# Optimization experiments

Measured on AMD Instinct MI355X. Metric: run time of the kernel, lower is better.

## Reference

```python
import jax, jax.numpy as jnp
import numpy as np

TEMPERATURE = 0.07
EPS = 1e-12  # F.normalize default eps


def setup_inputs() -> dict:
    key = jax.random.key(0)
    k1, k2, k3 = jax.random.split(key, 3)
    B, C, H, W = 2, 128, 256, 256
    return {
        "z1": jax.random.normal(k1, (B, C, H, W), dtype=jnp.float32),
        "z2": jax.random.normal(k2, (B, C, H, W), dtype=jnp.float32),
        "labels": jax.random.randint(k3, (B, H, W), 0, 5),
        "chunks": 64,
    }


def _l2_normalize(x, axis):
    n = jnp.sqrt(jnp.sum(x * x, axis=axis, keepdims=True))
    return x / jnp.maximum(n, EPS)


def reference(z1, z2, labels, chunks):
    B, C, H, W = z1.shape
    N = H * W
    M = N // chunks  # chunk length (N divisible by chunks)

    # normalize over channel dim, flatten spatial, split into chunks: [B, C, K, M]
    z1c = _l2_normalize(z1, axis=1).reshape(B, C, N).reshape(B, C, chunks, M)
    z2c = _l2_normalize(z2, axis=1).reshape(B, C, N).reshape(B, C, chunks, M)
    lab = labels.reshape(B, N).reshape(B, chunks, M)  # [B, K, M]

    # positives: cosine sim between matching chunks of z1 and z2 (unit vectors -> dot)
    pos = jnp.einsum("bckm,bckm->bkm", z1c, z2c) / TEMPERATURE  # [B, K, M]

    # negatives: in the source, (reps2, l2) after the j-loop are the LAST chunk of z2
    reps2_last = z2c[:, :, -1, :]  # [B, C, M]
    l2_last = lab[:, -1, :]        # [B, M]

    neg = jnp.einsum("bckm,bcn->bkmn", z1c, reps2_last)  # [B, K, M, M]
    mask = (lab[:, :, :, None] != l2_last[:, None, None, :])  # True where labels differ
    neg = neg * mask / TEMPERATURE

    logits = jnp.concatenate([pos[..., None], neg], axis=-1)  # [B, K, M, M+1]
    logp = jax.nn.log_softmax(logits, axis=-1)

    # per-(b,chunk) term is -mean over [M, M+1]; final is mean over B*chunks terms
    return -jnp.mean(logp)
```

## Files before the change

kernel.cpp:

```cpp
#include <hip/hip_runtime.h>
#include <hip/hip_bf16.h>

constexpr int BB = 2;
constexpr int CC = 128;
constexpr int NN = 65536;
constexpr int MM = 1024;
constexpr int LASTOFF = 63 * 1024;
constexpr float INV_T = 1.0f / 0.07f;
constexpr float L2E = 1.44269504088896340736f;
constexpr float C2 = INV_T * L2E;
constexpr float SCALE = 1.0f / (134348800.0f * 1.44269504088896340736f);

typedef float f32x4 __attribute__((ext_vector_type(4)));
typedef short bf16x8 __attribute__((ext_vector_type(8)));

__device__ __forceinline__ uint pack_bf16(float a, float b) {
  __hip_bfloat16 ha = __float2bfloat16(a);
  __hip_bfloat16 hb = __float2bfloat16(b);
  ushort ua = *reinterpret_cast<ushort*>(&ha);
  ushort ub = *reinterpret_cast<ushort*>(&hb);
  return (uint)ua | ((uint)ub << 16);
}

__global__ __launch_bounds__(256) void k_prep(
    const float* __restrict__ z1, const float* __restrict__ z2,
    uint* __restrict__ z1n, float* __restrict__ posv) {
  __shared__ float t1[64 * 129];
  __shared__ float part[3][8][65];
  __shared__ float inv1s[64];
  const int b = blockIdx.y;
  const int p0 = blockIdx.x * 64;
  const int t = threadIdx.x;
  const int p2 = t & 31;
  const int q = t >> 5;
  const float* s1 = z1 + (size_t)b * CC * NN + p0 + 2 * p2;
  const float* s2 = z2 + (size_t)b * CC * NN + p0 + 2 * p2;
  float a11 = 0.f, a22 = 0.f, a12 = 0.f;
  float b11 = 0.f, b22 = 0.f, b12 = 0.f;
#pragma unroll
  for (int e = 0; e < 16; e++) {
    int c = e * 8 + q;
    float2 x = *reinterpret_cast<const float2*>(s1 + (size_t)c * NN);
    float2 y = *reinterpret_cast<const float2*>(s2 + (size_t)c * NN);
    t1[(2 * p2) * 129 + c] = x.x;
    t1[(2 * p2 + 1) * 129 + c] = x.y;
    a11 += x.x * x.x; a22 += y.x * y.x; a12 += x.x * y.x;
    b11 += x.y * x.y; b22 += y.y * y.y; b12 += x.y * y.y;
  }
  part[0][q][2 * p2] = a11; part[0][q][2 * p2 + 1] = b11;
  part[1][q][2 * p2] = a22; part[1][q][2 * p2 + 1] = b22;
  part[2][q][2 * p2] = a12; part[2][q][2 * p2 + 1] = b12;
  __syncthreads();
  if (t < 64) {
    float s11 = 0.f, s22 = 0.f, s12 = 0.f;
#pragma unroll
    for (int qq = 0; qq < 8; qq++) {
      s11 += part[0][qq][t];
      s22 += part[1][qq][t];
      s12 += part[2][qq][t];
    }
    float i1 = 1.0f / fmaxf(sqrtf(s11), 1e-12f);
    float i2 = 1.0f / fmaxf(sqrtf(s22), 1e-12f);
    inv1s[t] = i1;
    posv[(size_t)b * NN + p0 + t] = s12 * i1 * i2 * INV_T;
  }
  __syncthreads();
  const size_t obase = ((size_t)b * NN + p0) * 64;
#pragma unroll
  for (int e = 0; e < 16; e++) {
    int lin = e * 256 + t;
    int pp = lin >> 6;
    int cp = lin & 63;
    float i1 = inv1s[pp];
    float v0 = t1[pp * 129 + 2 * cp] * i1;
    float v1 = t1[pp * 129 + 2 * cp + 1] * i1;
    z1n[obase + (size_t)pp * 64 + cp] = pack_bf16(v0, v1);
  }
}

__global__ __launch_bounds__(256) void k_r2(
    const float* __restrict__ z2, uint* __restrict__ r2n) {
  __shared__ float t2[64 * 129];
  __shared__ float part[8][65];
  __shared__ float inv2s[64];
  const int b = blockIdx.y;
  const int pg = blockIdx.x * 64;
  const int p0 = LASTOFF + pg;
  const int t = threadIdx.x;
  const int p2 = t & 31;
  const int q = t >> 5;
  const float* s2 = z2 + (size_t)b * CC * NN + p0 + 2 * p2;
  float a22 = 0.f, b22 = 0.f;
#pragma unroll
  for (int e = 0; e < 16; e++) {
    int c = e * 8 + q;
    float2 y = *reinterpret_cast<const float2*>(s2 + (size_t)c * NN);
    t2[(2 * p2) * 129 + c] = y.x;
    t2[(2 * p2 + 1) * 129 + c] = y.y;
    a22 += y.x * y.x;
    b22 += y.y * y.y;
  }
  part[q][2 * p2] = a22;
  part[q][2 * p2 + 1] = b22;
  __syncthreads();
  if (t < 64) {
    float s22 = 0.f;
#pragma unroll
    for (int qq = 0; qq < 8; qq++) s22 += part[qq][t];
    inv2s[t] = 1.0f / fmaxf(sqrtf(s22), 1e-12f);
  }
  __syncthreads();
  const size_t obase = ((size_t)b * MM + pg) * 64;
#pragma unroll
  for (int e = 0; e < 16; e++) {
    int lin = e * 256 + t;
    int pp = lin >> 6;
    int cp = lin & 63;
    float i2 = inv2s[pp];
    float v0 = t2[pp * 129 + 2 * cp] * i2;
    float v1 = t2[pp * 129 + 2 * cp + 1] * i2;
    r2n[obase + (size_t)pp * 64 + cp] = pack_bf16(v0, v1);
  }
}

__global__ __launch_bounds__(256, 2) void k_gemm(
    const ushort* __restrict__ z1n,
    const ushort* __restrict__ r2n,
    const int* __restrict__ lab,
    const float* __restrict__ posv,
    float* __restrict__ accum) {
  const int b = blockIdx.y;
  const int tid = threadIdx.x;
  const int w = tid >> 6;
  const int lane = tid & 63;
  const int r = lane & 15;
  const int kg = lane >> 4;
  const int wrow0 = blockIdx.x * 256 + w * 64;

  const ushort* Abase = z1n + ((size_t)b * NN + wrow0) * CC;
  bf16x8 av[4][4];
#pragma unroll
  for (int g = 0; g < 4; g++)
#pragma unroll
    for (int kk = 0; kk < 4; kk++)
      av[g][kk] = *reinterpret_cast<const bf16x8*>(
          Abase + ((size_t)(g * 16 + r)) * CC + kg * 8 + kk * 32);

  int rl[16];
#pragma unroll
  for (int g = 0; g < 4; g++)
#pragma unroll
    for (int i = 0; i < 4; i++)
      rl[g * 4 + i] = lab[(size_t)b * NN + wrow0 + g * 16 + kg * 4 + i];

  float sAcc[16], xAcc[16];
#pragma unroll
  for (int s = 0; s < 16; s++) { sAcc[s] = 0.f; xAcc[s] = 0.f; }

  const ushort* Bbase = r2n + (size_t)b * MM * CC;
  const int* clbase = lab + (size_t)b * NN + LASTOFF;

#pragma unroll 1
  for (int ch = 0; ch < 16; ch++) {
    const int n0 = ch * 64;
    bf16x8 bv[4][4];
#pragma unroll
    for (int tt = 0; tt < 4; tt++)
#pragma unroll
      for (int kk = 0; kk < 4; kk++)
        bv[tt][kk] = *reinterpret_cast<const bf16x8*>(
            Bbase + ((size_t)(n0 + tt * 16 + r)) * CC + kg * 8 + kk * 32);
    int cl[4];
#pragma unroll
    for (int tt = 0; tt < 4; tt++)
      cl[tt] = clbase[n0 + tt * 16 + r];

    f32x4 acc[4][4];
#pragma unroll
    for (int g = 0; g < 4; g++)
#pragma unroll
      for (int tt = 0; tt < 4; tt++)
        acc[g][tt] = f32x4{0.f, 0.f, 0.f, 0.f};

#pragma unroll
    for (int kk = 0; kk < 4; kk++)
#pragma unroll
      for (int g = 0; g < 4; g++)
#pragma unroll
        for (int tt = 0; tt < 4; tt++)
          acc[g][tt] = __builtin_amdgcn_mfma_f32_16x16x32_bf16(
              av[g][kk], bv[tt][kk], acc[g][tt], 0, 0, 0);

#pragma unroll
    for (int g = 0; g < 4; g++)
#pragma unroll
      for (int tt = 0; tt < 4; tt++)
#pragma unroll
        for (int i = 0; i < 4; i++) {
          float xm = acc[g][tt][i] * C2;
          float e = exp2f(xm);
          bool sel = (rl[g * 4 + i] != cl[tt]);
          sAcc[g * 4 + i] += sel ? e : 1.0f;
          xAcc[g * 4 + i] += sel ? xm : 0.0f;
        }
  }

#pragma unroll
  for (int d = 1; d < 16; d <<= 1) {
#pragma unroll
    for (int s = 0; s < 16; s++) {
      sAcc[s] += __shfl_xor(sAcc[s], d);
      xAcc[s] += __shfl_xor(xAcc[s], d);
    }
  }

  float tv = 0.f;
  if (r == 0) {
#pragma unroll
    for (int g = 0; g < 4; g++)
#pragma unroll
      for (int i = 0; i < 4; i++) {
        int row = wrow0 + g * 16 + kg * 4 + i;
        float pv = posv[(size_t)b * NN + row] * L2E;
        float s = sAcc[g * 4 + i] + exp2f(pv);
        float x = xAcc[g * 4 + i] + pv;
        tv += 1025.0f * __log2f(s) - x;
      }
  }
  tv += __shfl_xor(tv, 16);
  tv += __shfl_xor(tv, 32);
  if (lane == 0) atomicAdd(accum, tv);
}

__global__ void k_final(const float* __restrict__ accum, float* __restrict__ out) {
  out[0] = accum[0] * SCALE;
}

extern "C" void kernel_launch(void* const* d_in, const int* in_sizes, int n_in,
                              void* d_out, int out_size, void* d_ws, size_t ws_size,
                              hipStream_t stream) {
  const float* z1 = (const float*)d_in[0];
  const float* z2 = (const float*)d_in[1];
  const int* lab = (const int*)d_in[2];

  char* ws = (char*)d_ws;
  uint* z1n = (uint*)ws;
  uint* r2n = (uint*)(ws + 33554432);
  float* posv = (float*)(ws + 34078720);
  float* accum = (float*)(ws + 34603008);

  hipMemsetAsync(accum, 0, sizeof(float), stream);

  k_prep<<<dim3(NN / 64, BB), 256, 0, stream>>>(z1, z2, z1n, posv);
  k_r2<<<dim3(MM / 64, BB), 256, 0, stream>>>(z2, r2n);
  k_gemm<<<dim3(NN / 256, BB), 256, 0, stream>>>(
      (const ushort*)z1n, (const ushort*)r2n, lab, posv, accum);
  k_final<<<1, 1, 0, stream>>>(accum, (float*)d_out);
}
```

Measured before the change: 256.1 us.

## Normalize z1 inside GEMM and compute masked logit sum via per-label class sums

The bf16 normalized z1 buffer is dropped. A lighter k_pos kernel now computes only the inverse norms and positive logits, and k_gemm reads raw z1, normalizes and transposes it through LDS itself. The per-row sum of masked negative logits is computed algebraically: each class gets a precomputed z2 sum vector over columns with a different label, and one small extra MFMA multiplies it by the row, replacing the per-element xAcc accumulation. The inner loop also folds the temperature scale into the norms and uses the raw exp2 intrinsic. This removes a large intermediate write/read and some per-element ALU work, at the cost of a bigger LDS footprint in the GEMM, lower occupancy, and some bf16 rounding of the class sums.

```diff
diff --git a/kernel.cpp b/kernel.cpp
--- a/kernel.cpp
+++ b/kernel.cpp
@@ -10,6 +10,7 @@
 constexpr float L2E = 1.44269504088896340736f;
 constexpr float C2 = INV_T * L2E;
 constexpr float SCALE = 1.0f / (134348800.0f * 1.44269504088896340736f);
+constexpr float EPSN = 1e-12f;
 
 typedef float f32x4 __attribute__((ext_vector_type(4)));
 typedef short bf16x8 __attribute__((ext_vector_type(8)));
@@ -22,67 +23,39 @@
   return (uint)ua | ((uint)ub << 16);
 }
 
-__global__ __launch_bounds__(256) void k_prep(
+__global__ __launch_bounds__(256) void k_pos(
     const float* __restrict__ z1, const float* __restrict__ z2,
-    uint* __restrict__ z1n, float* __restrict__ posv) {
-  __shared__ float t1[64 * 129];
-  __shared__ float part[3][8][65];
-  __shared__ float inv1s[64];
+    float* __restrict__ i1c2, float* __restrict__ posv) {
   const int b = blockIdx.y;
-  const int p0 = blockIdx.x * 64;
-  const int t = threadIdx.x;
-  const int p2 = t & 31;
-  const int q = t >> 5;
-  const float* s1 = z1 + (size_t)b * CC * NN + p0 + 2 * p2;
-  const float* s2 = z2 + (size_t)b * CC * NN + p0 + 2 * p2;
-  float a11 = 0.f, a22 = 0.f, a12 = 0.f;
-  float b11 = 0.f, b22 = 0.f, b12 = 0.f;
-#pragma unroll
-  for (int e = 0; e < 16; e++) {
-    int c = e * 8 + q;
-    float2 x = *reinterpret_cast<const float2*>(s1 + (size_t)c * NN);
-    float2 y = *reinterpret_cast<const float2*>(s2 + (size_t)c * NN);
-    t1[(2 * p2) * 129 + c] = x.x;
-    t1[(2 * p2 + 1) * 129 + c] = x.y;
-    a11 += x.x * x.x; a22 += y.x * y.x; a12 += x.x * y.x;
-    b11 += x.y * x.y; b22 += y.y * y.y; b12 += x.y * y.y;
-  }
-  part[0][q][2 * p2] = a11; part[0][q][2 * p2 + 1] = b11;
-  part[1][q][2 * p2] = a22; part[1][q][2 * p2 + 1] = b22;
-  part[2][q][2 * p2] = a12; part[2][q][2 * p2 + 1] = b12;
-  __syncthreads();
-  if (t < 64) {
-    float s11 = 0.f, s22 = 0.f, s12 = 0.f;
-#pragma unroll
-    for (int qq = 0; qq < 8; qq++) {
-      s11 += part[0][qq][t];
-      s22 += part[1][qq][t];
-      s12 += part[2][qq][t];
-    }
-    float i1 = 1.0f / fmaxf(sqrtf(s11), 1e-12f);
-    float i2 = 1.0f / fmaxf(sqrtf(s22), 1e-12f);
-    inv1s[t] = i1;
-    posv[(size_t)b * NN + p0 + t] = s12 * i1 * i2 * INV_T;
-  }
-  __syncthreads();
-  const size_t obase = ((size_t)b * NN + p0) * 64;
-#pragma unroll
-  for (int e = 0; e < 16; e++) {
-    int lin = e * 256 + t;
-    int pp = lin >> 6;
-    int cp = lin & 63;
-    float i1 = inv1s[pp];
-    float v0 = t1[pp * 129 + 2 * cp] * i1;
-    float v1 = t1[pp * 129 + 2 * cp + 1] * i1;
-    z1n[obase + (size_t)pp * 64 + cp] = pack_bf16(v0, v1);
-  }
+  const int px = blockIdx.x * 512 + 2 * threadIdx.x;
+  const float* p1 = z1 + (size_t)b * CC * NN + px;
+  const float* p2 = z2 + (size_t)b * CC * NN + px;
+  float s11a = 0.f, s22a = 0.f, s12a = 0.f;
+  float s11b = 0.f, s22b = 0.f, s12b = 0.f;
+#pragma unroll 8
+  for (int c = 0; c < CC; c++) {
+    float2 x = *reinterpret_cast<const float2*>(p1 + (size_t)c * NN);
+    float2 y = *reinterpret_cast<const float2*>(p2 + (size_t)c * NN);
+    s11a += x.x * x.x; s22a += y.x * y.x; s12a += x.x * y.x;
+    s11b += x.y * x.y; s22b += y.y * y.y; s12b += x.y * y.y;
+  }
+  float i1a = 1.0f / fmaxf(sqrtf(s11a), EPSN);
+  float i2a = 1.0f / fmaxf(sqrtf(s22a), EPSN);
+  float i1b = 1.0f / fmaxf(sqrtf(s11b), EPSN);
+  float i2b = 1.0f / fmaxf(sqrtf(s22b), EPSN);
+  float2 iv = {i1a * C2, i1b * C2};
+  float2 pv = {s12a * i1a * i2a * C2, s12b * i1b * i2b * C2};
+  *reinterpret_cast<float2*>(i1c2 + (size_t)b * NN + px) = iv;
+  *reinterpret_cast<float2*>(posv + (size_t)b * NN + px) = pv;
 }
 
 __global__ __launch_bounds__(256) void k_r2(
-    const float* __restrict__ z2, uint* __restrict__ r2n) {
+    const float* __restrict__ z2, const int* __restrict__ lab,
+    uint* __restrict__ r2n, float* __restrict__ Sv) {
   __shared__ float t2[64 * 129];
   __shared__ float part[8][65];
   __shared__ float inv2s[64];
+  __shared__ int cls[64];
   const int b = blockIdx.y;
   const int pg = blockIdx.x * 64;
   const int p0 = LASTOFF + pg;
@@ -107,7 +80,8 @@
     float s22 = 0.f;
 #pragma unroll
     for (int qq = 0; qq < 8; qq++) s22 += part[qq][t];
-    inv2s[t] = 1.0f / fmaxf(sqrtf(s22), 1e-12f);
+    inv2s[t] = 1.0f / fmaxf(sqrtf(s22), EPSN);
+    cls[t] = lab[(size_t)b * NN + p0 + t];
   }
   __syncthreads();
   const size_t obase = ((size_t)b * MM + pg) * 64;
@@ -121,41 +95,90 @@
     float v1 = t2[pp * 129 + 2 * cp + 1] * i2;
     r2n[obase + (size_t)pp * 64 + cp] = pack_bf16(v0, v1);
   }
-}
-
-__global__ __launch_bounds__(256, 2) void k_gemm(
-    const ushort* __restrict__ z1n,
-    const ushort* __restrict__ r2n,
-    const int* __restrict__ lab,
-    const float* __restrict__ posv,
+  const int c = t & 127;
+  const int h = t >> 7;
+  float tot = 0.f, se0 = 0.f, se1 = 0.f, se2 = 0.f, se3 = 0.f, se4 = 0.f;
+#pragma unroll
+  for (int k = 0; k < 32; k++) {
+    int pp = h * 32 + k;
+    float val = t2[pp * 129 + c] * inv2s[pp];
+    int lb = cls[pp];
+    tot += val;
+    se0 += (lb == 0) ? val : 0.f;
+    se1 += (lb == 1) ? val : 0.f;
+    se2 += (lb == 2) ? val : 0.f;
+    se3 += (lb == 3) ? val : 0.f;
+    se4 += (lb == 4) ? val : 0.f;
+  }
+  float* svb = Sv + b * 640 + c;
+  atomicAdd(svb + 0 * 128, tot - se0);
+  atomicAdd(svb + 1 * 128, tot - se1);
+  atomicAdd(svb + 2 * 128, tot - se2);
+  atomicAdd(svb + 3 * 128, tot - se3);
+  atomicAdd(svb + 4 * 128, tot - se4);
+}
+
+__global__ void k_svpack(const float* __restrict__ Sv, ushort* __restrict__ r2x) {
+  int i = blockIdx.x * 256 + threadIdx.x;
+  if (i >= BB * 16 * 128) return;
+  int b = i >> 11, rr = (i >> 7) & 15, c = i & 127;
+  float v = (rr < 5) ? Sv[b * 640 + rr * 128 + c] : 0.0f;
+  __hip_bfloat16 h = __float2bfloat16(v);
+  r2x[i] = *reinterpret_cast<ushort*>(&h);
+}
+
+__global__ __launch_bounds__(256) void k_gemm(
+    const float* __restrict__ z1, const float* __restrict__ i1c2,
+    const ushort* __restrict__ r2n, const ushort* __restrict__ r2x,
+    const int* __restrict__ lab, const float* __restrict__ posv,
     float* __restrict__ accum) {
+  __shared__ ushort At[128 * 258];
   const int b = blockIdx.y;
+  const int px0 = blockIdx.x * 256;
   const int tid = threadIdx.x;
   const int w = tid >> 6;
   const int lane = tid & 63;
   const int r = lane & 15;
   const int kg = lane >> 4;
-  const int wrow0 = blockIdx.x * 256 + w * 64;
-
-  const ushort* Abase = z1n + ((size_t)b * NN + wrow0) * CC;
+
+  {
+    const float* zb = z1 + (size_t)b * CC * NN + px0 + 4 * lane;
+    f32x4 iv = *reinterpret_cast<const f32x4*>(i1c2 + (size_t)b * NN + px0 + 4 * lane);
+#pragma unroll 4
+    for (int e = 0; e < 32; e++) {
+      int c = w * 32 + e;
+      f32x4 v = *reinterpret_cast<const f32x4*>(zb + (size_t)c * NN);
+      uint2 uu;
+      uu.x = pack_bf16(v[0] * iv[0], v[1] * iv[1]);
+      uu.y = pack_bf16(v[2] * iv[2], v[3] * iv[3]);
+      *reinterpret_cast<uint2*>(&At[c * 258 + 4 * lane]) = uu;
+    }
+  }
+  __syncthreads();
+
+  const int wrow0 = w * 64;
   bf16x8 av[4][4];
 #pragma unroll
   for (int g = 0; g < 4; g++)
 #pragma unroll
-    for (int kk = 0; kk < 4; kk++)
-      av[g][kk] = *reinterpret_cast<const bf16x8*>(
-          Abase + ((size_t)(g * 16 + r)) * CC + kg * 8 + kk * 32);
+    for (int kk = 0; kk < 4; kk++) {
+      bf16x8 tv;
+#pragma unroll
+      for (int j = 0; j < 8; j++)
+        tv[j] = (short)At[(kg * 8 + kk * 32 + j) * 258 + wrow0 + g * 16 + r];
+      av[g][kk] = tv;
+    }
 
   int rl[16];
 #pragma unroll
   for (int g = 0; g < 4; g++)
 #pragma unroll
     for (int i = 0; i < 4; i++)
-      rl[g * 4 + i] = lab[(size_t)b * NN + wrow0 + g * 16 + kg * 4 + i];
-
-  float sAcc[16], xAcc[16];
-#pragma unroll
-  for (int s = 0; s < 16; s++) { sAcc[s] = 0.f; xAcc[s] = 0.f; }
+      rl[g * 4 + i] = lab[(size_t)b * NN + px0 + wrow0 + g * 16 + kg * 4 + i];
+
+  float sAcc[16];
+#pragma unroll
+  for (int s = 0; s < 16; s++) sAcc[s] = 0.f;
 
   const ushort* Bbase = r2n + (size_t)b * MM * CC;
   const int* clbase = lab + (size_t)b * NN + LASTOFF;
@@ -197,22 +220,39 @@
       for (int tt = 0; tt < 4; tt++)
 #pragma unroll
         for (int i = 0; i < 4; i++) {
-          float xm = acc[g][tt][i] * C2;
-          float e = exp2f(xm);
-          bool sel = (rl[g * 4 + i] != cl[tt]);
-          sAcc[g * 4 + i] += sel ? e : 1.0f;
-          xAcc[g * 4 + i] += sel ? xm : 0.0f;
+          float xm = (rl[g * 4 + i] != cl[tt]) ? acc[g][tt][i] : 0.0f;
+          sAcc[g * 4 + i] += __builtin_amdgcn_exp2f(xm);
         }
   }
 
-#pragma unroll
-  for (int d = 1; d < 16; d <<= 1) {
-#pragma unroll
-    for (int s = 0; s < 16; s++) {
-      sAcc[s] += __shfl_xor(sAcc[s], d);
-      xAcc[s] += __shfl_xor(xAcc[s], d);
+  f32x4 accx[4];
+  {
+    bf16x8 bx[4];
+#pragma unroll
+    for (int kk = 0; kk < 4; kk++)
+      bx[kk] = *reinterpret_cast<const bf16x8*>(
+          r2x + (size_t)b * 16 * CC + (size_t)r * CC + kg * 8 + kk * 32);
+#pragma unroll
+    for (int g = 0; g < 4; g++) {
+      accx[g] = f32x4{0.f, 0.f, 0.f, 0.f};
+#pragma unroll
+      for (int kk = 0; kk < 4; kk++)
+        accx[g] = __builtin_amdgcn_mfma_f32_16x16x32_bf16(
+            av[g][kk], bx[kk], accx[g], 0, 0, 0);
     }
   }
+
+#pragma unroll
+  for (int d = 1; d < 16; d <<= 1)
+#pragma unroll
+    for (int s = 0; s < 16; s++) sAcc[s] += __shfl_xor(sAcc[s], d);
+
+  float xsel[16];
+#pragma unroll
+  for (int g = 0; g < 4; g++)
+#pragma unroll
+    for (int i = 0; i < 4; i++)
+      xsel[g * 4 + i] = __shfl(accx[g][i], (lane & 48) | rl[g * 4 + i]);
 
   float tv = 0.f;
   if (r == 0) {
@@ -220,10 +260,10 @@
     for (int g = 0; g < 4; g++)
 #pragma unroll
       for (int i = 0; i < 4; i++) {
-        int row = wrow0 + g * 16 + kg * 4 + i;
-        float pv = posv[(size_t)b * NN + row] * L2E;
-        float s = sAcc[g * 4 + i] + exp2f(pv);
-        float x = xAcc[g * 4 + i] + pv;
+        int row = px0 + wrow0 + g * 16 + kg * 4 + i;
+        float pv = posv[(size_t)b * NN + row];
+        float s = sAcc[g * 4 + i] + __builtin_amdgcn_exp2f(pv);
+        float x = xsel[g * 4 + i] + pv;
         tv += 1025.0f * __log2f(s) - x;
       }
   }
@@ -232,7 +272,7 @@
   if (lane == 0) atomicAdd(accum, tv);
 }
 
-__global__ void k_final(const float* __restrict__ accum, float* __restrict__ out) {
+__global__ void k_scale(const float* __restrict__ accum, float* __restrict__ out) {
   out[0] = accum[0] * SCALE;
 }
 
@@ -244,16 +284,19 @@
   const int* lab = (const int*)d_in[2];
 
   char* ws = (char*)d_ws;
-  uint* z1n = (uint*)ws;
-  uint* r2n = (uint*)(ws + 33554432);
-  float* posv = (float*)(ws + 34078720);
-  float* accum = (float*)(ws + 34603008);
-
-  hipMemsetAsync(accum, 0, sizeof(float), stream);
-
-  k_prep<<<dim3(NN / 64, BB), 256, 0, stream>>>(z1, z2, z1n, posv);
-  k_r2<<<dim3(MM / 64, BB), 256, 0, stream>>>(z2, r2n);
+  uint* r2n   = (uint*)ws;
+  ushort* r2x = (ushort*)(ws + 524288);
+  float* posv = (float*)(ws + 532480);
+  float* i1c2 = (float*)(ws + 1056768);
+  float* Sv   = (float*)(ws + 1581056);
+  float* accum = (float*)(ws + 1586176);
+
+  hipMemsetAsync(ws + 1581056, 0, 5124, stream);
+
+  k_pos<<<dim3(NN / 512, BB), 256, 0, stream>>>(z1, z2, i1c2, posv);
+  k_r2<<<dim3(MM / 64, BB), 256, 0, stream>>>(z2, lab, r2n, Sv);
+  k_svpack<<<dim3(16), 256, 0, stream>>>(Sv, r2x);
   k_gemm<<<dim3(NN / 256, BB), 256, 0, stream>>>(
-      (const ushort*)z1n, (const ushort*)r2n, lab, posv, accum);
-  k_final<<<1, 1, 0, stream>>>(accum, (float*)d_out);
-}
+      z1, i1c2, (const ushort*)r2n, r2x, lab, posv, accum);
+  k_scale<<<1, 1, 0, stream>>>(accum, (float*)d_out);
+}
```

After: 253.6 us. Within noise of the previous version (-1.0%).
